# Kernel tuning notes

Hardware: AMD Instinct MI355X
Metric: run time of the kernel (lower is better)

The kernel has to match this reference:

```python
import jax, jax.numpy as jnp
import numpy as np

N_NODES = 100000
N_EDGES = 640000
IN_FEAT = 128
HID_FEAT = 128
OUT_FEAT = 40


def sage_conv(x, src, dst, W_l, W_r, b, n_nodes):
    # PyG SAGEConv (aggr='mean', root_weight=True):
    #   out_i = W_l @ mean_{j in N(i)} x_j + W_r @ x_i + b
    msg = x[src]  # [E, d] gather
    agg = jax.ops.segment_sum(msg, dst, num_segments=n_nodes)  # [N, d]
    cnt = jax.ops.segment_sum(jnp.ones((src.shape[0],), x.dtype), dst,
                              num_segments=n_nodes)
    agg = agg / jnp.maximum(cnt, 1.0)[:, None]  # segment mean
    return agg @ W_l + x @ W_r + b


def setup_inputs() -> dict:
    key = jax.random.key(0)
    ks = jax.random.split(key, 8)
    s = lambda fan_in: 1.0 / np.sqrt(fan_in)
    x = jax.random.normal(ks[0], (N_NODES, IN_FEAT), jnp.float32)
    edge_index = jax.random.randint(ks[1], (2, N_EDGES), 0, N_NODES, jnp.int64)
    W1l = jax.random.normal(ks[2], (IN_FEAT, HID_FEAT), jnp.float32) * s(IN_FEAT)
    W1r = jax.random.normal(ks[3], (IN_FEAT, HID_FEAT), jnp.float32) * s(IN_FEAT)
    b1 = jnp.zeros((HID_FEAT,), jnp.float32)
    W2l = jax.random.normal(ks[4], (HID_FEAT, OUT_FEAT), jnp.float32) * s(HID_FEAT)
    W2r = jax.random.normal(ks[5], (HID_FEAT, OUT_FEAT), jnp.float32) * s(HID_FEAT)
    b2 = jnp.zeros((OUT_FEAT,), jnp.float32)
    return {"x": x, "edge_index": edge_index, "W1l": W1l, "W1r": W1r,
            "b1": b1, "W2l": W2l, "W2r": W2r, "b2": b2}


def reference(x, edge_index, W1l, W1r, b1, W2l, W2r, b2):
    src, dst = edge_index[0], edge_index[1]
    n = x.shape[0]
    h = jax.nn.relu(sage_conv(x, src, dst, W1l, W1r, b1, n))
    # dropout is identity in eval mode
    out = sage_conv(h, src, dst, W2l, W2r, b2, n)
    return jax.nn.log_softmax(out, axis=1)
```

## Files before the change

kernel.cpp:

```cpp
#include <hip/hip_runtime.h>
#include <math.h>

#define NN 100000
#define NE 640000
#define DF 128
#define DOUT 40
#define D2 48

typedef short bf16x8 __attribute__((ext_vector_type(8)));
typedef float f32x4 __attribute__((ext_vector_type(4)));
typedef float f32x2 __attribute__((ext_vector_type(2)));

#if defined(__has_builtin)
#if __has_builtin(__builtin_amdgcn_cvt_pk_f32_fp8) && __has_builtin(__builtin_amdgcn_cvt_pk_fp8_f32)
#define HW_FP8 1
#endif
#endif
#ifndef HW_FP8
#define HW_FP8 0
#endif

__device__ __forceinline__ unsigned short f2bf(float f) {
    unsigned int u = __float_as_uint(f);
    u += 0x7fffu + ((u >> 16) & 1u);
    return (unsigned short)(u >> 16);
}
__device__ __forceinline__ float bf2f(unsigned short u) {
    return __uint_as_float((unsigned int)u << 16);
}

__device__ __forceinline__ unsigned int f2fp8_manual(float f) {
    unsigned u = __float_as_uint(f);
    unsigned s = (u >> 24) & 0x80u;
    unsigned au = u & 0x7fffffffu;
    if (au > 0x43e00000u) au = 0x43e00000u;
    au += 0x7ffffu + ((au >> 20) & 1u);
    if (au < 0x3c800000u) return s;
    unsigned e = (au >> 23) - 120u;
    return s | (e << 3) | ((au >> 20) & 7u);
}

__device__ __forceinline__ unsigned short f2fp8x2(float x, float y) {
#if HW_FP8
    int v = __builtin_amdgcn_cvt_pk_fp8_f32(x, y, 0, false);
    return (unsigned short)(v & 0xffff);
#else
    return (unsigned short)(f2fp8_manual(x) | (f2fp8_manual(y) << 8));
#endif
}

__device__ __forceinline__ void fp8pair(unsigned short p, float& x, float& y) {
#if HW_FP8
    f32x2 r = __builtin_amdgcn_cvt_pk_f32_fp8((int)(unsigned)p, false);
    x = r.x; y = r.y;
#else
    unsigned lo = p & 0xffu, hi = (p >> 8) & 0xffu;
    x = __uint_as_float(((lo & 0x80u) << 24) | ((lo & 0x7fu) << 20)) * 0x1.0p120f;
    y = __uint_as_float(((hi & 0x80u) << 24) | ((hi & 0x7fu) << 20)) * 0x1.0p120f;
#endif
}

#define PREP_CONV 6250
#define PREP_W1   (PREP_CONV + 16)
#define PREP_W2   (PREP_W1 + 6)
#define PREP_GRID (PREP_W2 + 391)

__global__ __launch_bounds__(256) void prep_kernel(const float* __restrict__ x,
                                                   unsigned short* __restrict__ xb,
                                                   unsigned char* __restrict__ xq,
                                                   const float* __restrict__ W1l,
                                                   const float* __restrict__ W1r,
                                                   unsigned short* __restrict__ w1p,
                                                   const float* __restrict__ W2l,
                                                   const float* __restrict__ W2r,
                                                   unsigned short* __restrict__ w2lp,
                                                   unsigned short* __restrict__ w2rp,
                                                   int* __restrict__ deg) {
    const int bid = blockIdx.x;
    const int tid = threadIdx.x;
    if (bid < PREP_CONV) {
        int i = (bid * 256 + tid) * 8;
        float4 a = *reinterpret_cast<const float4*>(x + i);
        float4 b = *reinterpret_cast<const float4*>(x + i + 4);
        uint4 o;
        o.x = (unsigned)f2bf(a.x) | ((unsigned)f2bf(a.y) << 16);
        o.y = (unsigned)f2bf(a.z) | ((unsigned)f2bf(a.w) << 16);
        o.z = (unsigned)f2bf(b.x) | ((unsigned)f2bf(b.y) << 16);
        o.w = (unsigned)f2bf(b.z) | ((unsigned)f2bf(b.w) << 16);
        *reinterpret_cast<uint4*>(xb + (size_t)i) = o;
        unsigned short q0 = f2fp8x2(a.x, a.y);
        unsigned short q1 = f2fp8x2(a.z, a.w);
        unsigned short q2 = f2fp8x2(b.x, b.y);
        unsigned short q3 = f2fp8x2(b.z, b.w);
        uint2 qo;
        qo.x = (unsigned)q0 | ((unsigned)q1 << 16);
        qo.y = (unsigned)q2 | ((unsigned)q3 << 16);
        *reinterpret_cast<uint2*>(xq + (size_t)i) = qo;
    } else if (bid < PREP_W1) {
        int t = (bid - PREP_CONV) * 256 + tid;
        int lane = t & 63;
        int ct = (t >> 6) & 7;
        int kt = t >> 9;
        int c  = ct * 16 + (lane & 15);
        int k0 = (kt & 3) * 32 + (lane >> 4) * 8;
        const float* W = (kt < 4) ? W1l : W1r;
        unsigned int o[4];
#pragma unroll
        for (int j = 0; j < 4; ++j) {
            unsigned int lo = f2bf(W[(size_t)(k0 + 2 * j) * DF + c]);
            unsigned int hi = f2bf(W[(size_t)(k0 + 2 * j + 1) * DF + c]);
            o[j] = lo | (hi << 16);
        }
        uint4 v; v.x = o[0]; v.y = o[1]; v.z = o[2]; v.w = o[3];
        *reinterpret_cast<uint4*>(w1p + (size_t)t * 8) = v;
    } else if (bid < PREP_W2) {
        int t = (bid - PREP_W1) * 256 + tid;
        if (t < 1536) {
            int lane = t & 63;
            int g  = t >> 6;
            int ct = g % 3;
            int kt = g / 3;
            int c  = ct * 16 + (lane & 15);
            int k0 = (kt & 3) * 32 + (lane >> 4) * 8;
            const float* W = (kt < 4) ? W2l : W2r;
            unsigned short* dstp = (kt < 4) ? w2lp : w2rp;
            int slot = ((kt & 3) * 3 + ct) * 64 + lane;
            unsigned int o[4];
#pragma unroll
            for (int j = 0; j < 4; ++j) {
                unsigned int lo = (c < DOUT) ? f2bf(W[(size_t)(k0 + 2 * j) * DOUT + c]) : 0u;
                unsigned int hi = (c < DOUT) ? f2bf(W[(size_t)(k0 + 2 * j + 1) * DOUT + c]) : 0u;
                o[j] = lo | (hi << 16);
            }
            uint4 v; v.x = o[0]; v.y = o[1]; v.z = o[2]; v.w = o[3];
            *reinterpret_cast<uint4*>(dstp + (size_t)slot * 8) = v;
        }
    } else {
        int i = (bid - PREP_W2) * 256 + tid;
        if (i < NN) deg[i] = 0;
    }
}


__global__ __launch_bounds__(256) void hist_kernel(const int* __restrict__ dst,
                                                   int* __restrict__ deg,
                                                   int* __restrict__ rank) {
    int e = blockIdx.x * blockDim.x + threadIdx.x;
    if (e < NE) rank[e] = atomicAdd(&deg[dst[e]], 1);
}

__global__ __launch_bounds__(256) void scan_block_kernel(const int* __restrict__ deg,
                                                         int* __restrict__ loc,
                                                         int* __restrict__ part) {
    __shared__ int tmp[256];
    const int t = threadIdx.x;
    const int i = blockIdx.x * 256 + t;
    int v = (i < NN) ? deg[i] : 0;
    tmp[t] = v;
    __syncthreads();
    for (int off = 1; off < 256; off <<= 1) {
        int a = (t >= off) ? tmp[t - off] : 0;
        __syncthreads();
        tmp[t] += a;
        __syncthreads();
    }
    if (i < NN) loc[i] = tmp[t] - v;
    if (t == 255) part[blockIdx.x] = tmp[t];
}

__global__ __launch_bounds__(256) void add_off_kernel(const int* __restrict__ loc,
                                                      const int* __restrict__ part,
                                                      const int* __restrict__ deg,
                                                      int2* __restrict__ ofs2) {
    __shared__ int wsum[4];
    const int bb = blockIdx.x;
    const int t  = threadIdx.x;
    int psum = 0;
    for (int i = t; i < bb; i += 256) psum += part[i];
#pragma unroll
    for (int off = 32; off > 0; off >>= 1) psum += __shfl_down(psum, off);
    if ((t & 63) == 0) wsum[t >> 6] = psum;
    __syncthreads();
    int base = wsum[0] + wsum[1] + wsum[2] + wsum[3];
    int i = bb * 256 + t;
    if (i < NN) {
        int o = loc[i] + base;
        ofs2[i] = make_int2(o, o + deg[i]);
    }
}

__global__ __launch_bounds__(256) void fill_kernel(const int* __restrict__ src,
                                                   const int* __restrict__ dst,
                                                   const int2* __restrict__ ofs2,
                                                   const int* __restrict__ rank,
                                                   int* __restrict__ srcs) {
    int e = blockIdx.x * blockDim.x + threadIdx.x;
    if (e < NE) {
        int d = dst[e];
        srcs[ofs2[d].x + rank[e]] = src[e];
    }
}

__global__ __launch_bounds__(256) void gather_mean_fp8_kernel(const unsigned char* __restrict__ xq,
                                                              const int2* __restrict__ ofs2,
                                                              const int* __restrict__ srcs,
                                                              unsigned short* __restrict__ agg) {
    const int gid  = blockIdx.x * 256 + threadIdx.x;
    const int node = gid >> 6;
    const int lane = threadIdx.x & 63;
    if (node >= NN) return;
    const int2 be = ofs2[node];
    const int b = be.x;
    const int e = be.y;
    const unsigned char* fp = xq + lane * 2;

    float ax0 = 0.f, ay0 = 0.f, ax1 = 0.f, ay1 = 0.f;
    float ax2 = 0.f, ay2 = 0.f, ax3 = 0.f, ay3 = 0.f;

    for (int j = b; j < e; j += 8) {
        int s[8];
#pragma unroll
        for (int k = 0; k < 8; ++k)
            s[k] = (j + k < e) ? srcs[j + k] : -1;
        unsigned short v[8];
#pragma unroll
        for (int k = 0; k < 8; ++k)
            v[k] = ((unsigned)s[k] < (unsigned)NN)
                 ? *reinterpret_cast<const unsigned short*>(fp + (size_t)s[k] * DF) : (unsigned short)0;
        float dx, dy;
        fp8pair(v[0], dx, dy); ax0 += dx; ay0 += dy;
        fp8pair(v[1], dx, dy); ax1 += dx; ay1 += dy;
        fp8pair(v[2], dx, dy); ax2 += dx; ay2 += dy;
        fp8pair(v[3], dx, dy); ax3 += dx; ay3 += dy;
        fp8pair(v[4], dx, dy); ax0 += dx; ay0 += dy;
        fp8pair(v[5], dx, dy); ax1 += dx; ay1 += dy;
        fp8pair(v[6], dx, dy); ax2 += dx; ay2 += dy;
        fp8pair(v[7], dx, dy); ax3 += dx; ay3 += dy;
    }

    float ax = (ax0 + ax1) + (ax2 + ax3);
    float ay = (ay0 + ay1) + (ay2 + ay3);
    const float sc = 1.0f / fmaxf((float)(e - b), 1.0f);
    unsigned int o = (unsigned)f2bf(ax * sc) | ((unsigned)f2bf(ay * sc) << 16);
    *reinterpret_cast<unsigned int*>(agg + (size_t)node * DF + lane * 2) = o;
}

#define G_ROWS 64
#define LDSW 136

__global__ __launch_bounds__(256) void gemm1_kernel(const unsigned short* __restrict__ aggb,
                                                    const unsigned short* __restrict__ xb,
                                                    const unsigned short* __restrict__ w1p,
                                                    const unsigned short* __restrict__ w2lp,
                                                    const unsigned short* __restrict__ w2rp,
                                                    const float* __restrict__ b1,
                                                    const float* __restrict__ b2,
                                                    unsigned short* __restrict__ h2b,
                                                    unsigned short* __restrict__ h2rb) {
    __shared__ unsigned short sA[G_ROWS * LDSW];
    __shared__ unsigned short sX[G_ROWS * LDSW];
    const int t = threadIdx.x;
    const int row0 = blockIdx.x * G_ROWS;

    for (int i = t; i < G_ROWS * 16; i += 256) {
        int r = i >> 4, ch = i & 15;
        int sr = row0 + r; if (sr > NN - 1) sr = NN - 1;
        *reinterpret_cast<uint4*>(&sA[r * LDSW + ch * 8]) =
            *reinterpret_cast<const uint4*>(aggb + (size_t)sr * DF + ch * 8);
        *reinterpret_cast<uint4*>(&sX[r * LDSW + ch * 8]) =
            *reinterpret_cast<const uint4*>(xb + (size_t)sr * DF + ch * 8);
    }
    __syncthreads();

    const int lane = t & 63;
    const int w = t >> 6;
    const int lr = lane & 15;
    const int hi = lane >> 4;
    f32x4 acc[8];
#pragma unroll
    for (int i = 0; i < 8; ++i) acc[i] = (f32x4){0.f, 0.f, 0.f, 0.f};

    const int arow = (w * 16 + lr) * LDSW + hi * 8;
#pragma unroll
    for (int half = 0; half < 2; ++half) {
        const unsigned short* base = half ? sX : sA;
#pragma unroll
        for (int kq = 0; kq < 4; ++kq) {
            bf16x8 a = __builtin_bit_cast(bf16x8,
                *reinterpret_cast<const uint4*>(&base[arow + kq * 32]));
            const unsigned short* wp = w1p + (size_t)(((half * 4 + kq) * 8) * 64 + lane) * 8;
#pragma unroll
            for (int ct = 0; ct < 8; ++ct) {
                bf16x8 b = __builtin_bit_cast(bf16x8,
                    *reinterpret_cast<const uint4*>(wp + ct * 512));
                acc[ct] = __builtin_amdgcn_mfma_f32_16x16x32_bf16(a, b, acc[ct], 0, 0, 0);
            }
        }
    }

    unsigned short hreg[8][4];
#pragma unroll
    for (int ct = 0; ct < 8; ++ct) {
        float bias = b1[ct * 16 + lr];
#pragma unroll
        for (int v = 0; v < 4; ++v) {
            hreg[ct][v] = f2bf(fmaxf(acc[ct][v] + bias, 0.f));
        }
    }

    __syncthreads();
#pragma unroll
    for (int ct = 0; ct < 8; ++ct) {
#pragma unroll
        for (int v = 0; v < 4; ++v) {
            sA[(w * 16 + hi * 4 + v) * LDSW + ct * 16 + lr] = hreg[ct][v];
        }
    }
    __syncthreads();

    f32x4 acc2[3], acc3[3];
#pragma unroll
    for (int i = 0; i < 3; ++i) {
        acc2[i] = (f32x4){0.f, 0.f, 0.f, 0.f};
        acc3[i] = (f32x4){0.f, 0.f, 0.f, 0.f};
    }
#pragma unroll
    for (int kq = 0; kq < 4; ++kq) {
        bf16x8 a = __builtin_bit_cast(bf16x8,
            *reinterpret_cast<const uint4*>(&sA[arow + kq * 32]));
        const unsigned short* wpl = w2lp + (size_t)((kq * 3) * 64 + lane) * 8;
        const unsigned short* wpr = w2rp + (size_t)((kq * 3) * 64 + lane) * 8;
#pragma unroll
        for (int ct = 0; ct < 3; ++ct) {
            bf16x8 bl = __builtin_bit_cast(bf16x8,
                *reinterpret_cast<const uint4*>(wpl + ct * 512));
            bf16x8 br = __builtin_bit_cast(bf16x8,
                *reinterpret_cast<const uint4*>(wpr + ct * 512));
            acc2[ct] = __builtin_amdgcn_mfma_f32_16x16x32_bf16(a, bl, acc2[ct], 0, 0, 0);
            acc3[ct] = __builtin_amdgcn_mfma_f32_16x16x32_bf16(a, br, acc3[ct], 0, 0, 0);
        }
    }
#pragma unroll
    for (int ct = 0; ct < 3; ++ct) {
        int col = ct * 16 + lr;
        float bias2 = (col < DOUT) ? b2[col] : 0.f;
#pragma unroll
        for (int v = 0; v < 4; ++v) {
            int row = row0 + w * 16 + hi * 4 + v;
            if (row < NN) {
                h2b[(size_t)row * D2 + col]  = f2bf(acc2[ct][v]);
                h2rb[(size_t)row * D2 + col] = f2bf(acc3[ct][v] + bias2);
            }
        }
    }
}

__global__ __launch_bounds__(256) void gather_finish_kernel(const unsigned short* __restrict__ h2b,
                                                            const unsigned short* __restrict__ h2rb,
                                                            const int2* __restrict__ ofs2,
                                                            const int* __restrict__ srcs,
                                                            float* __restrict__ out) {
    const int gid   = blockIdx.x * 256 + threadIdx.x;
    const int node  = gid >> 5;
    const int lane32 = threadIdx.x & 31;
    if (node >= NN) return;
    const int2 be = ofs2[node];
    const int b = be.x;
    const int e = be.y;
    const bool act = lane32 < 20;
    const unsigned short* fp = h2b + lane32 * 2;

    float ax0 = 0.f, ay0 = 0.f, ax1 = 0.f, ay1 = 0.f;
    float ax2 = 0.f, ay2 = 0.f, ax3 = 0.f, ay3 = 0.f;

    for (int j = b; j < e; j += 8) {
        int s[8];
#pragma unroll
        for (int k = 0; k < 8; ++k)
            s[k] = (j + k < e) ? srcs[j + k] : -1;
        unsigned int v[8];
#pragma unroll
        for (int k = 0; k < 8; ++k)
            v[k] = (act && (unsigned)s[k] < (unsigned)NN)
                 ? *reinterpret_cast<const unsigned int*>(fp + (size_t)s[k] * D2) : 0u;
        ax0 += __uint_as_float(v[0] << 16);  ay0 += __uint_as_float(v[0] & 0xffff0000u);
        ax1 += __uint_as_float(v[1] << 16);  ay1 += __uint_as_float(v[1] & 0xffff0000u);
        ax2 += __uint_as_float(v[2] << 16);  ay2 += __uint_as_float(v[2] & 0xffff0000u);
        ax3 += __uint_as_float(v[3] << 16);  ay3 += __uint_as_float(v[3] & 0xffff0000u);
        ax0 += __uint_as_float(v[4] << 16);  ay0 += __uint_as_float(v[4] & 0xffff0000u);
        ax1 += __uint_as_float(v[5] << 16);  ay1 += __uint_as_float(v[5] & 0xffff0000u);
        ax2 += __uint_as_float(v[6] << 16);  ay2 += __uint_as_float(v[6] & 0xffff0000u);
        ax3 += __uint_as_float(v[7] << 16);  ay3 += __uint_as_float(v[7] & 0xffff0000u);
    }

    const float sc = 1.0f / fmaxf((float)(e - b), 1.0f);
    float a0 = ((ax0 + ax1) + (ax2 + ax3)) * sc;
    float a1 = ((ay0 + ay1) + (ay2 + ay3)) * sc;

    float lv0 = -INFINITY, lv1 = -INFINITY;
    if (act) {
        unsigned int sv = *reinterpret_cast<const unsigned int*>(h2rb + (size_t)node * D2 + lane32 * 2);
        lv0 = a0 + __uint_as_float(sv << 16);
        lv1 = a1 + __uint_as_float(sv & 0xffff0000u);
    }

    float mx = fmaxf(lv0, lv1);
#pragma unroll
    for (int off = 16; off > 0; off >>= 1) mx = fmaxf(mx, __shfl_xor(mx, off));
    float e0 = act ? __expf(lv0 - mx) : 0.f;
    float e1 = act ? __expf(lv1 - mx) : 0.f;
    float s = e0 + e1;
#pragma unroll
    for (int off = 16; off > 0; off >>= 1) s += __shfl_xor(s, off);
    float lz = mx + __logf(s);
    if (act) {
        float2 o = make_float2(lv0 - lz, lv1 - lz);
        *reinterpret_cast<float2*>(out + (size_t)node * DOUT + lane32 * 2) = o;
    }
}

extern "C" void kernel_launch(void* const* d_in, const int* in_sizes, int n_in,
                              void* d_out, int out_size, void* d_ws, size_t ws_size,
                              hipStream_t stream) {
    const float* x   = (const float*)d_in[0];
    const int*   ei  = (const int*)d_in[1];
    const int*   src = ei;
    const int*   dst = ei + NE;
    const float* W1l = (const float*)d_in[2];
    const float* W1r = (const float*)d_in[3];
    const float* b1  = (const float*)d_in[4];
    const float* W2l = (const float*)d_in[5];
    const float* W2r = (const float*)d_in[6];
    const float* b2  = (const float*)d_in[7];
    float* out = (float*)d_out;

    int* ip    = (int*)d_ws;
    int* deg   = ip;
    int* loc   = ip + 100000;
    int* rank  = ip + 200000;
    int* srcs  = ip + 840000;
    int* part  = ip + 1480008;
    int2* ofs2 = (int2*)(ip + 1480520);
    unsigned short* up    = (unsigned short*)(ip + 1680520);
    unsigned short* xb    = up;
    unsigned short* aggb  = up + 12800000;
    unsigned short* h2b   = up + 25600000;
    unsigned short* h2rb  = up + 30400000;
    unsigned short* w1p   = up + 35200000;
    unsigned short* w2lp  = up + 35232768;
    unsigned short* w2rp  = up + 35238912;
    unsigned char*  xq    = (unsigned char*)(up + 35245056);

    prep_kernel<<<PREP_GRID, 256, 0, stream>>>(x, xb, xq, W1l, W1r, w1p,
                                               W2l, W2r, w2lp, w2rp, deg);

    hist_kernel<<<(NE + 255) / 256, 256, 0, stream>>>(dst, deg, rank);
    scan_block_kernel<<<391, 256, 0, stream>>>(deg, loc, part);
    add_off_kernel<<<391, 256, 0, stream>>>(loc, part, deg, ofs2);
    fill_kernel<<<(NE + 255) / 256, 256, 0, stream>>>(src, dst, ofs2, rank, srcs);

    gather_mean_fp8_kernel<<<25000, 256, 0, stream>>>(xq, ofs2, srcs, aggb);
    gemm1_kernel<<<1563, 256, 0, stream>>>(aggb, xb, w1p, w2lp, w2rp, b1, b2, h2b, h2rb);
    gather_finish_kernel<<<12500, 256, 0, stream>>>(h2b, h2rb, ofs2, srcs, out);
}
```

Before: 153.6 us.

## Fuse first-layer neighbor mean gather into GEMM1 kernel via LDS

```diff
diff --git a/kernel.cpp b/kernel.cpp
--- a/kernel.cpp
+++ b/kernel.cpp
@@ -24,9 +24,6 @@
     unsigned int u = __float_as_uint(f);
     u += 0x7fffu + ((u >> 16) & 1u);
     return (unsigned short)(u >> 16);
-}
-__device__ __forceinline__ float bf2f(unsigned short u) {
-    return __uint_as_float((unsigned int)u << 16);
 }
 
 __device__ __forceinline__ unsigned int f2fp8_manual(float f) {
@@ -201,100 +198,97 @@
     }
 }
 
-__global__ __launch_bounds__(256) void gather_mean_fp8_kernel(const unsigned char* __restrict__ xq,
-                                                              const int2* __restrict__ ofs2,
-                                                              const int* __restrict__ srcs,
-                                                              unsigned short* __restrict__ agg) {
-    const int gid  = blockIdx.x * 256 + threadIdx.x;
-    const int node = gid >> 6;
-    const int lane = threadIdx.x & 63;
-    if (node >= NN) return;
-    const int2 be = ofs2[node];
-    const int b = be.x;
-    const int e = be.y;
-    const unsigned char* fp = xq + lane * 2;
-
-    float ax0 = 0.f, ay0 = 0.f, ax1 = 0.f, ay1 = 0.f;
-    float ax2 = 0.f, ay2 = 0.f, ax3 = 0.f, ay3 = 0.f;
-
-    for (int j = b; j < e; j += 8) {
-        int s[8];
-#pragma unroll
-        for (int k = 0; k < 8; ++k)
-            s[k] = (j + k < e) ? srcs[j + k] : -1;
-        unsigned short v[8];
-#pragma unroll
-        for (int k = 0; k < 8; ++k)
-            v[k] = ((unsigned)s[k] < (unsigned)NN)
-                 ? *reinterpret_cast<const unsigned short*>(fp + (size_t)s[k] * DF) : (unsigned short)0;
-        float dx, dy;
-        fp8pair(v[0], dx, dy); ax0 += dx; ay0 += dy;
-        fp8pair(v[1], dx, dy); ax1 += dx; ay1 += dy;
-        fp8pair(v[2], dx, dy); ax2 += dx; ay2 += dy;
-        fp8pair(v[3], dx, dy); ax3 += dx; ay3 += dy;
-        fp8pair(v[4], dx, dy); ax0 += dx; ay0 += dy;
-        fp8pair(v[5], dx, dy); ax1 += dx; ay1 += dy;
-        fp8pair(v[6], dx, dy); ax2 += dx; ay2 += dy;
-        fp8pair(v[7], dx, dy); ax3 += dx; ay3 += dy;
-    }
-
-    float ax = (ax0 + ax1) + (ax2 + ax3);
-    float ay = (ay0 + ay1) + (ay2 + ay3);
-    const float sc = 1.0f / fmaxf((float)(e - b), 1.0f);
-    unsigned int o = (unsigned)f2bf(ax * sc) | ((unsigned)f2bf(ay * sc) << 16);
-    *reinterpret_cast<unsigned int*>(agg + (size_t)node * DF + lane * 2) = o;
-}
-
 #define G_ROWS 64
 #define LDSW 136
 
-__global__ __launch_bounds__(256) void gemm1_kernel(const unsigned short* __restrict__ aggb,
-                                                    const unsigned short* __restrict__ xb,
-                                                    const unsigned short* __restrict__ w1p,
-                                                    const unsigned short* __restrict__ w2lp,
-                                                    const unsigned short* __restrict__ w2rp,
-                                                    const float* __restrict__ b1,
-                                                    const float* __restrict__ b2,
-                                                    unsigned short* __restrict__ h2b,
-                                                    unsigned short* __restrict__ h2rb) {
+__global__ __launch_bounds__(256) void gemm1_fused_kernel(const unsigned char* __restrict__ xq,
+                                                          const unsigned short* __restrict__ xb,
+                                                          const int2* __restrict__ ofs2,
+                                                          const int* __restrict__ srcs,
+                                                          const unsigned short* __restrict__ w1p,
+                                                          const unsigned short* __restrict__ w2lp,
+                                                          const unsigned short* __restrict__ w2rp,
+                                                          const float* __restrict__ b1,
+                                                          const float* __restrict__ b2,
+                                                          unsigned short* __restrict__ h2b,
+                                                          unsigned short* __restrict__ h2rb) {
     __shared__ unsigned short sA[G_ROWS * LDSW];
-    __shared__ unsigned short sX[G_ROWS * LDSW];
     const int t = threadIdx.x;
-    const int row0 = blockIdx.x * G_ROWS;
-
-    for (int i = t; i < G_ROWS * 16; i += 256) {
-        int r = i >> 4, ch = i & 15;
-        int sr = row0 + r; if (sr > NN - 1) sr = NN - 1;
-        *reinterpret_cast<uint4*>(&sA[r * LDSW + ch * 8]) =
-            *reinterpret_cast<const uint4*>(aggb + (size_t)sr * DF + ch * 8);
-        *reinterpret_cast<uint4*>(&sX[r * LDSW + ch * 8]) =
-            *reinterpret_cast<const uint4*>(xb + (size_t)sr * DF + ch * 8);
-    }
-    __syncthreads();
-
     const int lane = t & 63;
     const int w = t >> 6;
+    const int row0 = blockIdx.x * G_ROWS;
+
+    const unsigned char* fp = xq + lane * 2;
+    for (int i = 0; i < 16; ++i) {
+        const int node = row0 + w * 16 + i;
+        float ax0 = 0.f, ay0 = 0.f, ax1 = 0.f, ay1 = 0.f;
+        float ax2 = 0.f, ay2 = 0.f, ax3 = 0.f, ay3 = 0.f;
+        float sc = 0.f;
+        if (node < NN) {
+            const int2 be = ofs2[node];
+            const int b = be.x, e = be.y;
+            for (int j = b; j < e; j += 8) {
+                int s[8];
+#pragma unroll
+                for (int k = 0; k < 8; ++k)
+                    s[k] = (j + k < e) ? srcs[j + k] : -1;
+                unsigned short v[8];
+#pragma unroll
+                for (int k = 0; k < 8; ++k)
+                    v[k] = ((unsigned)s[k] < (unsigned)NN)
+                         ? *reinterpret_cast<const unsigned short*>(fp + (size_t)s[k] * DF)
+                         : (unsigned short)0;
+                float dx, dy;
+                fp8pair(v[0], dx, dy); ax0 += dx; ay0 += dy;
+                fp8pair(v[1], dx, dy); ax1 += dx; ay1 += dy;
+                fp8pair(v[2], dx, dy); ax2 += dx; ay2 += dy;
+                fp8pair(v[3], dx, dy); ax3 += dx; ay3 += dy;
+                fp8pair(v[4], dx, dy); ax0 += dx; ay0 += dy;
+                fp8pair(v[5], dx, dy); ax1 += dx; ay1 += dy;
+                fp8pair(v[6], dx, dy); ax2 += dx; ay2 += dy;
+                fp8pair(v[7], dx, dy); ax3 += dx; ay3 += dy;
+            }
+            sc = 1.0f / fmaxf((float)(e - b), 1.0f);
+        }
+        float ax = ((ax0 + ax1) + (ax2 + ax3)) * sc;
+        float ay = ((ay0 + ay1) + (ay2 + ay3)) * sc;
+        unsigned int o = (unsigned)f2bf(ax) | ((unsigned)f2bf(ay) << 16);
+        *reinterpret_cast<unsigned int*>(&sA[(w * 16 + i) * LDSW + lane * 2]) = o;
+    }
+    __syncthreads();
+
     const int lr = lane & 15;
     const int hi = lane >> 4;
+    const int arow = (w * 16 + lr) * LDSW + hi * 8;
+    int xrow = row0 + w * 16 + lr; if (xrow > NN - 1) xrow = NN - 1;
+    const unsigned short* xrp = xb + (size_t)xrow * DF + hi * 8;
+
     f32x4 acc[8];
 #pragma unroll
     for (int i = 0; i < 8; ++i) acc[i] = (f32x4){0.f, 0.f, 0.f, 0.f};
 
-    const int arow = (w * 16 + lr) * LDSW + hi * 8;
-#pragma unroll
-    for (int half = 0; half < 2; ++half) {
-        const unsigned short* base = half ? sX : sA;
-#pragma unroll
-        for (int kq = 0; kq < 4; ++kq) {
-            bf16x8 a = __builtin_bit_cast(bf16x8,
-                *reinterpret_cast<const uint4*>(&base[arow + kq * 32]));
-            const unsigned short* wp = w1p + (size_t)(((half * 4 + kq) * 8) * 64 + lane) * 8;
-#pragma unroll
-            for (int ct = 0; ct < 8; ++ct) {
-                bf16x8 b = __builtin_bit_cast(bf16x8,
-                    *reinterpret_cast<const uint4*>(wp + ct * 512));
-                acc[ct] = __builtin_amdgcn_mfma_f32_16x16x32_bf16(a, b, acc[ct], 0, 0, 0);
-            }
+#pragma unroll
+    for (int kq = 0; kq < 4; ++kq) {
+        bf16x8 a = __builtin_bit_cast(bf16x8,
+            *reinterpret_cast<const uint4*>(&sA[arow + kq * 32]));
+        const unsigned short* wp = w1p + (size_t)((kq * 8) * 64 + lane) * 8;
+#pragma unroll
+        for (int ct = 0; ct < 8; ++ct) {
+            bf16x8 b = __builtin_bit_cast(bf16x8,
+                *reinterpret_cast<const uint4*>(wp + ct * 512));
+            acc[ct] = __builtin_amdgcn_mfma_f32_16x16x32_bf16(a, b, acc[ct], 0, 0, 0);
+        }
+    }
+#pragma unroll
+    for (int kq = 0; kq < 4; ++kq) {
+        bf16x8 a = __builtin_bit_cast(bf16x8,
+            *reinterpret_cast<const uint4*>(xrp + kq * 32));
+        const unsigned short* wp = w1p + (size_t)(((4 + kq) * 8) * 64 + lane) * 8;
+#pragma unroll
+        for (int ct = 0; ct < 8; ++ct) {
+            bf16x8 b = __builtin_bit_cast(bf16x8,
+                *reinterpret_cast<const uint4*>(wp + ct * 512));
+            acc[ct] = __builtin_amdgcn_mfma_f32_16x16x32_bf16(a, b, acc[ct], 0, 0, 0);
         }
     }
 
@@ -443,13 +437,12 @@
     int2* ofs2 = (int2*)(ip + 1480520);
     unsigned short* up    = (unsigned short*)(ip + 1680520);
     unsigned short* xb    = up;
-    unsigned short* aggb  = up + 12800000;
-    unsigned short* h2b   = up + 25600000;
-    unsigned short* h2rb  = up + 30400000;
-    unsigned short* w1p   = up + 35200000;
-    unsigned short* w2lp  = up + 35232768;
-    unsigned short* w2rp  = up + 35238912;
-    unsigned char*  xq    = (unsigned char*)(up + 35245056);
+    unsigned short* h2b   = up + 12800000;
+    unsigned short* h2rb  = up + 17600000;
+    unsigned short* w1p   = up + 22400000;
+    unsigned short* w2lp  = up + 22432768;
+    unsigned short* w2rp  = up + 22438912;
+    unsigned char*  xq    = (unsigned char*)(up + 22445056);
 
     prep_kernel<<<PREP_GRID, 256, 0, stream>>>(x, xb, xq, W1l, W1r, w1p,
                                                W2l, W2r, w2lp, w2rp, deg);
@@ -459,7 +452,7 @@
     add_off_kernel<<<391, 256, 0, stream>>>(loc, part, deg, ofs2);
     fill_kernel<<<(NE + 255) / 256, 256, 0, stream>>>(src, dst, ofs2, rank, srcs);
 
-    gather_mean_fp8_kernel<<<25000, 256, 0, stream>>>(xq, ofs2, srcs, aggb);
-    gemm1_kernel<<<1563, 256, 0, stream>>>(aggb, xb, w1p, w2lp, w2rp, b1, b2, h2b, h2rb);
+    gemm1_fused_kernel<<<1563, 256, 0, stream>>>(xq, xb, ofs2, srcs,
+                                                 w1p, w2lp, w2rp, b1, b2, h2b, h2rb);
     gather_finish_kernel<<<12500, 256, 0, stream>>>(h2b, h2rb, ofs2, srcs, out);
 }
```

Result: slower. 165.2 us (+7.6%).

## Fuse degree histogram into prep kernel and widen fp8 gather to 4 bytes per lane

Applied to the files above, without the earlier changes.

```diff
diff --git a/kernel.cpp b/kernel.cpp
--- a/kernel.cpp
+++ b/kernel.cpp
@@ -24,9 +24,6 @@
     unsigned int u = __float_as_uint(f);
     u += 0x7fffu + ((u >> 16) & 1u);
     return (unsigned short)(u >> 16);
-}
-__device__ __forceinline__ float bf2f(unsigned short u) {
-    return __uint_as_float((unsigned int)u << 16);
 }
 
 __device__ __forceinline__ unsigned int f2fp8_manual(float f) {
@@ -60,12 +57,30 @@
 #endif
 }
 
-#define PREP_CONV 6250
-#define PREP_W1   (PREP_CONV + 16)
-#define PREP_W2   (PREP_W1 + 6)
-#define PREP_GRID (PREP_W2 + 391)
-
-__global__ __launch_bounds__(256) void prep_kernel(const float* __restrict__ x,
+__device__ __forceinline__ void fp8quad(unsigned int q, float& x0, float& y0,
+                                        float& x1, float& y1) {
+#if HW_FP8
+    f32x2 lo = __builtin_amdgcn_cvt_pk_f32_fp8((int)q, false);
+    f32x2 hi = __builtin_amdgcn_cvt_pk_f32_fp8((int)q, true);
+    x0 = lo.x; y0 = lo.y; x1 = hi.x; y1 = hi.y;
+#else
+    fp8pair((unsigned short)(q & 0xffffu), x0, y0);
+    fp8pair((unsigned short)(q >> 16), x1, y1);
+#endif
+}
+
+__global__ __launch_bounds__(256) void zero_deg_kernel(int* __restrict__ deg) {
+    int i = blockIdx.x * 256 + threadIdx.x;
+    if (i < NN) deg[i] = 0;
+}
+
+#define MK_HIST 2500
+#define MK_CONV (MK_HIST + 6250)
+#define MK_W1   (MK_CONV + 16)
+#define MK_W2   (MK_W1 + 6)
+#define MK_GRID MK_W2
+
+__global__ __launch_bounds__(256) void mega_kernel(const float* __restrict__ x,
                                                    unsigned short* __restrict__ xb,
                                                    unsigned char* __restrict__ xq,
                                                    const float* __restrict__ W1l,
@@ -75,11 +90,16 @@
                                                    const float* __restrict__ W2r,
                                                    unsigned short* __restrict__ w2lp,
                                                    unsigned short* __restrict__ w2rp,
-                                                   int* __restrict__ deg) {
+                                                   const int* __restrict__ dst,
+                                                   int* __restrict__ deg,
+                                                   int* __restrict__ rank) {
     const int bid = blockIdx.x;
     const int tid = threadIdx.x;
-    if (bid < PREP_CONV) {
-        int i = (bid * 256 + tid) * 8;
+    if (bid < MK_HIST) {
+        int e = bid * 256 + tid;
+        if (e < NE) rank[e] = atomicAdd(&deg[dst[e]], 1);
+    } else if (bid < MK_CONV) {
+        int i = ((bid - MK_HIST) * 256 + tid) * 8;
         float4 a = *reinterpret_cast<const float4*>(x + i);
         float4 b = *reinterpret_cast<const float4*>(x + i + 4);
         uint4 o;
@@ -96,8 +116,8 @@
         qo.x = (unsigned)q0 | ((unsigned)q1 << 16);
         qo.y = (unsigned)q2 | ((unsigned)q3 << 16);
         *reinterpret_cast<uint2*>(xq + (size_t)i) = qo;
-    } else if (bid < PREP_W1) {
-        int t = (bid - PREP_CONV) * 256 + tid;
+    } else if (bid < MK_W1) {
+        int t = (bid - MK_CONV) * 256 + tid;
         int lane = t & 63;
         int ct = (t >> 6) & 7;
         int kt = t >> 9;
@@ -113,8 +133,8 @@
         }
         uint4 v; v.x = o[0]; v.y = o[1]; v.z = o[2]; v.w = o[3];
         *reinterpret_cast<uint4*>(w1p + (size_t)t * 8) = v;
-    } else if (bid < PREP_W2) {
-        int t = (bid - PREP_W1) * 256 + tid;
+    } else {
+        int t = (bid - MK_W1) * 256 + tid;
         if (t < 1536) {
             int lane = t & 63;
             int g  = t >> 6;
@@ -135,19 +155,9 @@
             uint4 v; v.x = o[0]; v.y = o[1]; v.z = o[2]; v.w = o[3];
             *reinterpret_cast<uint4*>(dstp + (size_t)slot * 8) = v;
         }
-    } else {
-        int i = (bid - PREP_W2) * 256 + tid;
-        if (i < NN) deg[i] = 0;
-    }
-}
-
-
-__global__ __launch_bounds__(256) void hist_kernel(const int* __restrict__ dst,
-                                                   int* __restrict__ deg,
-                                                   int* __restrict__ rank) {
-    int e = blockIdx.x * blockDim.x + threadIdx.x;
-    if (e < NE) rank[e] = atomicAdd(&deg[dst[e]], 1);
-}
+    }
+}
+
 
 __global__ __launch_bounds__(256) void scan_block_kernel(const int* __restrict__ deg,
                                                          int* __restrict__ loc,
@@ -205,44 +215,46 @@
                                                               const int2* __restrict__ ofs2,
                                                               const int* __restrict__ srcs,
                                                               unsigned short* __restrict__ agg) {
-    const int gid  = blockIdx.x * 256 + threadIdx.x;
-    const int node = gid >> 6;
-    const int lane = threadIdx.x & 63;
+    const int gid    = blockIdx.x * 256 + threadIdx.x;
+    const int node   = gid >> 5;
+    const int lane32 = threadIdx.x & 31;
     if (node >= NN) return;
     const int2 be = ofs2[node];
     const int b = be.x;
     const int e = be.y;
-    const unsigned char* fp = xq + lane * 2;
-
-    float ax0 = 0.f, ay0 = 0.f, ax1 = 0.f, ay1 = 0.f;
-    float ax2 = 0.f, ay2 = 0.f, ax3 = 0.f, ay3 = 0.f;
+    const unsigned char* fp = xq + lane32 * 4;
+
+    float a0 = 0.f, a1 = 0.f, a2 = 0.f, a3 = 0.f;
+    float c0 = 0.f, c1 = 0.f, c2 = 0.f, c3 = 0.f;
 
     for (int j = b; j < e; j += 8) {
         int s[8];
 #pragma unroll
         for (int k = 0; k < 8; ++k)
             s[k] = (j + k < e) ? srcs[j + k] : -1;
-        unsigned short v[8];
+        unsigned int v[8];
 #pragma unroll
         for (int k = 0; k < 8; ++k)
             v[k] = ((unsigned)s[k] < (unsigned)NN)
-                 ? *reinterpret_cast<const unsigned short*>(fp + (size_t)s[k] * DF) : (unsigned short)0;
-        float dx, dy;
-        fp8pair(v[0], dx, dy); ax0 += dx; ay0 += dy;
-        fp8pair(v[1], dx, dy); ax1 += dx; ay1 += dy;
-        fp8pair(v[2], dx, dy); ax2 += dx; ay2 += dy;
-        fp8pair(v[3], dx, dy); ax3 += dx; ay3 += dy;
-        fp8pair(v[4], dx, dy); ax0 += dx; ay0 += dy;
-        fp8pair(v[5], dx, dy); ax1 += dx; ay1 += dy;
-        fp8pair(v[6], dx, dy); ax2 += dx; ay2 += dy;
-        fp8pair(v[7], dx, dy); ax3 += dx; ay3 += dy;
-    }
-
-    float ax = (ax0 + ax1) + (ax2 + ax3);
-    float ay = (ay0 + ay1) + (ay2 + ay3);
+                 ? *reinterpret_cast<const unsigned int*>(fp + (size_t)s[k] * DF) : 0u;
+        float x0, y0, x1, y1;
+        fp8quad(v[0], x0, y0, x1, y1); a0 += x0; a1 += y0; a2 += x1; a3 += y1;
+        fp8quad(v[1], x0, y0, x1, y1); c0 += x0; c1 += y0; c2 += x1; c3 += y1;
+        fp8quad(v[2], x0, y0, x1, y1); a0 += x0; a1 += y0; a2 += x1; a3 += y1;
+        fp8quad(v[3], x0, y0, x1, y1); c0 += x0; c1 += y0; c2 += x1; c3 += y1;
+        fp8quad(v[4], x0, y0, x1, y1); a0 += x0; a1 += y0; a2 += x1; a3 += y1;
+        fp8quad(v[5], x0, y0, x1, y1); c0 += x0; c1 += y0; c2 += x1; c3 += y1;
+        fp8quad(v[6], x0, y0, x1, y1); a0 += x0; a1 += y0; a2 += x1; a3 += y1;
+        fp8quad(v[7], x0, y0, x1, y1); c0 += x0; c1 += y0; c2 += x1; c3 += y1;
+    }
+
     const float sc = 1.0f / fmaxf((float)(e - b), 1.0f);
-    unsigned int o = (unsigned)f2bf(ax * sc) | ((unsigned)f2bf(ay * sc) << 16);
-    *reinterpret_cast<unsigned int*>(agg + (size_t)node * DF + lane * 2) = o;
+    float s0 = (a0 + c0) * sc, s1 = (a1 + c1) * sc;
+    float s2 = (a2 + c2) * sc, s3 = (a3 + c3) * sc;
+    uint2 o;
+    o.x = (unsigned)f2bf(s0) | ((unsigned)f2bf(s1) << 16);
+    o.y = (unsigned)f2bf(s2) | ((unsigned)f2bf(s3) << 16);
+    *reinterpret_cast<uint2*>(agg + (size_t)node * DF + lane32 * 4) = o;
 }
 
 #define G_ROWS 64
@@ -451,15 +463,15 @@
     unsigned short* w2rp  = up + 35238912;
     unsigned char*  xq    = (unsigned char*)(up + 35245056);
 
-    prep_kernel<<<PREP_GRID, 256, 0, stream>>>(x, xb, xq, W1l, W1r, w1p,
-                                               W2l, W2r, w2lp, w2rp, deg);
-
-    hist_kernel<<<(NE + 255) / 256, 256, 0, stream>>>(dst, deg, rank);
+    zero_deg_kernel<<<391, 256, 0, stream>>>(deg);
+    mega_kernel<<<MK_GRID, 256, 0, stream>>>(x, xb, xq, W1l, W1r, w1p,
+                                             W2l, W2r, w2lp, w2rp, dst, deg, rank);
+
     scan_block_kernel<<<391, 256, 0, stream>>>(deg, loc, part);
     add_off_kernel<<<391, 256, 0, stream>>>(loc, part, deg, ofs2);
     fill_kernel<<<(NE + 255) / 256, 256, 0, stream>>>(src, dst, ofs2, rank, srcs);
 
-    gather_mean_fp8_kernel<<<25000, 256, 0, stream>>>(xq, ofs2, srcs, aggb);
+    gather_mean_fp8_kernel<<<12500, 256, 0, stream>>>(xq, ofs2, srcs, aggb);
     gemm1_kernel<<<1563, 256, 0, stream>>>(aggb, xb, w1p, w2lp, w2rp, b1, b2, h2b, h2rb);
     gather_finish_kernel<<<12500, 256, 0, stream>>>(h2b, h2rb, ofs2, srcs, out);
 }
```

Result: faster. 148.1 us, median of 2 (-3.6%).
